# Optimization experiments

Hardware: AMD Instinct MI355X
Metric: run time of the kernel (lower is better)

## Reference

```python
import jax, jax.numpy as jnp
import numpy as np

DIM = 192
NUM_HEADS = 6
WS = (2, 8, 8)          # (wd, wh, ww)
SHIFT = (1, 4, 4)
B, D, H, W = 2, 4, 128, 128
N_WIN_TOK = WS[0] * WS[1] * WS[2]   # 128
NW = (D // WS[0]) * (H // WS[1]) * (W // WS[2])  # 512 windows per sample


def _rel_pos_index(ws):
    d, h, w = ws
    coords = np.stack(np.meshgrid(np.arange(d), np.arange(h), np.arange(w), indexing='ij'))
    cf = coords.reshape(3, -1)
    rel = (cf[:, :, None] - cf[:, None, :]).transpose(1, 2, 0).astype(np.int64)
    rel[:, :, 0] += d - 1
    rel[:, :, 1] += h - 1
    rel[:, :, 2] += w - 1
    rel[:, :, 0] *= (2 * h - 1) * (2 * w - 1)
    rel[:, :, 1] *= 2 * w - 1
    return rel.sum(-1)  # (N, N)

REL_IDX = _rel_pos_index(WS)


def _sine_pos(HW, num_pos_feats, temperature=10000.0):
    # matches get_sine_position_encoding(normalize=True)
    scale = 2 * np.pi
    eps = 1e-6
    ones = np.ones((1, HW[0], HW[1]), np.float32)
    y = ones.cumsum(1)
    x = ones.cumsum(2)
    y = y / (y[:, -1:, :] + eps) * scale
    x = x / (x[:, :, -1:] + eps) * scale
    i = np.arange(num_pos_feats, dtype=np.float32)
    dim_t = temperature ** (2.0 * np.floor(i / 2) / num_pos_feats)
    px = x[:, :, :, None] / dim_t
    py = y[:, :, :, None] / dim_t
    px = np.stack((np.sin(px[..., 0::2]), np.cos(px[..., 1::2])), axis=4).reshape(1, HW[0], HW[1], -1)
    py = np.stack((np.sin(py[..., 0::2]), np.cos(py[..., 1::2])), axis=4).reshape(1, HW[0], HW[1], -1)
    pos = np.concatenate((py, px), axis=3)  # (1, H, W, 2*npf)
    return pos.reshape(1, HW[0] * HW[1], -1)

POS_BIAS = _sine_pos((WS[1], WS[2]), DIM // 2)  # (1, 64, DIM)


def _ln(x, w, b):
    mu = x.mean(-1, keepdims=True)
    var = x.var(-1, keepdims=True)
    return (x - mu) / jnp.sqrt(var + 1e-5) * w + b


def _qkv(x, w, b):
    B_, N, C = x.shape
    y = (x @ w.T + b).reshape(B_, N, 3, NUM_HEADS, C // NUM_HEADS).transpose(2, 0, 3, 1, 4)
    return y[0], y[1], y[2]  # each (B_, h, N, hd)


def _attn(q, k, v, mask, rpb=None):
    # q,k,v: (B_, h, N, hd); mask: (nW, N, N) or None; rpb: (h, N, N) or None
    scale = q.shape[-1] ** -0.5
    a = jnp.einsum('bhnd,bhmd->bhnm', q * scale, k)
    if rpb is not None:
        a = a + rpb[None]
    if mask is not None:
        B_, h, N, _ = a.shape
        nW = mask.shape[0]
        a = (a.reshape(B_ // nW, nW, h, N, N) + mask[None, :, None]).reshape(B_, h, N, N)
    a = jax.nn.softmax(a, axis=-1)
    out = jnp.einsum('bhnm,bhmd->bhnd', a, v)
    B_, h, N, hd = out.shape
    return out.transpose(0, 2, 1, 3).reshape(B_, N, h * hd)


def setup_inputs() -> dict:
    key = jax.random.key(0)
    ks = jax.random.split(key, 8)
    C = DIM
    hid = int(C * 2.0)
    f = lambda k, shp: jax.random.normal(k, shp, jnp.float32) * 0.02
    tbl = (2 * WS[0] - 1) * (2 * WS[1] - 1) * (2 * WS[2] - 1)
    return {
        'x': jax.random.normal(ks[0], (B, D, H, W, C), jnp.float32),
        'mask_matrix': jnp.zeros((NW, N_WIN_TOK, N_WIN_TOK), jnp.float32),
        'norm1_w': jnp.ones((C,), jnp.float32), 'norm1_b': jnp.zeros((C,), jnp.float32),
        'qkv_self_w': f(ks[1], (3 * C, C)), 'qkv_self_b': jnp.zeros((3 * C,), jnp.float32),
        'qkv_mut_w': f(ks[2], (3 * C, C)), 'qkv_mut_b': jnp.zeros((3 * C,), jnp.float32),
        'rpb_table': f(ks[3], (tbl, NUM_HEADS)),
        'proj_w': f(ks[4], (C, 2 * C)), 'proj_b': jnp.zeros((C,), jnp.float32),
        'norm2_w': jnp.ones((C,), jnp.float32), 'norm2_b': jnp.zeros((C,), jnp.float32),
        'fc11_w': f(ks[5], (hid, C)), 'fc11_b': jnp.zeros((hid,), jnp.float32),
        'fc12_w': f(ks[6], (hid, C)), 'fc12_b': jnp.zeros((hid,), jnp.float32),
        'fc2_w': f(ks[7], (C, hid)), 'fc2_b': jnp.zeros((C,), jnp.float32),
    }


def reference(x, mask_matrix, norm1_w, norm1_b, qkv_self_w, qkv_self_b,
              qkv_mut_w, qkv_mut_b, rpb_table, proj_w, proj_b,
              norm2_w, norm2_b, fc11_w, fc11_b, fc12_w, fc12_b, fc2_w, fc2_b):
    Bb, Dd, Hh, Ww_, C = x.shape
    wd, wh, ww = WS
    N = wd * wh * ww
    Nh = N // 2

    # ---- part1: windowed mutual+self attention with cyclic shift ----
    h1 = _ln(x, norm1_w, norm1_b)
    sh = jnp.roll(h1, (-SHIFT[0], -SHIFT[1], -SHIFT[2]), axis=(1, 2, 3))
    # window_partition -> (B*nW, N, C)
    xw = sh.reshape(Bb, Dd // wd, wd, Hh // wh, wh, Ww_ // ww, ww, C)
    xw = xw.transpose(0, 1, 3, 5, 2, 4, 6, 7).reshape(-1, N, C)

    # self-attention with relative position bias
    q, k, v = _qkv(xw, qkv_self_w, qkv_self_b)
    rpb = rpb_table[REL_IDX.reshape(-1)].reshape(N, N, NUM_HEADS).transpose(2, 0, 1)
    x_self = _attn(q, k, v, mask_matrix[:, :N, :N], rpb)  # (B_, N, C)

    # mutual attention (no relative bias), sine positional bias added to input
    pos = jnp.tile(jnp.asarray(POS_BIAS, x.dtype), (1, 2, 1))  # (1, N, C)
    q, k, v = _qkv(xw + pos, qkv_mut_w, qkv_mut_b)
    q1, q2 = q[:, :, :Nh], q[:, :, Nh:]
    k1, k2 = k[:, :, :Nh], k[:, :, Nh:]
    v1, v2 = v[:, :, :Nh], v[:, :, Nh:]
    m2 = mask_matrix[:, :Nh, :Nh]
    x1 = _attn(q2, k1, v1, m2)  # frame2 queries attend frame1
    x2 = _attn(q1, k2, v2, m2)
    x_out = jnp.concatenate([jnp.concatenate([x1, x2], axis=1), x_self], axis=2)  # (B_, N, 2C)
    xp = x_out @ proj_w.T + proj_b  # (B_, N, C)

    # window_reverse + roll back
    rev = xp.reshape(Bb, Dd // wd, Hh // wh, Ww_ // ww, wd, wh, ww, C)
    rev = rev.transpose(0, 1, 4, 2, 5, 3, 6, 7).reshape(Bb, Dd, Hh, Ww_, C)
    rev = jnp.roll(rev, SHIFT, axis=(1, 2, 3))
    x = x + rev

    # ---- part2: GEGLU MLP ----
    h2 = _ln(x, norm2_w, norm2_b)
    mlp = (jax.nn.gelu(h2 @ fc11_w.T + fc11_b, approximate=False) * (h2 @ fc12_w.T + fc12_b)) @ fc2_w.T + fc2_b
    return x + mlp
```

## Files before the change

kernel.cpp:

```cpp
#include <hip/hip_runtime.h>
#include <hip/hip_bf16.h>

typedef __hip_bfloat16 bf16;
typedef __attribute__((ext_vector_type(8))) short short8;
typedef __attribute__((ext_vector_type(4))) float f32x4;

#define NTOKENS 131072
#define MFMA __builtin_amdgcn_mfma_f32_16x16x32_bf16

static constexpr size_t A_OFF    = 0;
static constexpr size_t Q_OFF    = A_OFF   + (size_t)NTOKENS*192*2;
static constexpr size_t O_OFF    = Q_OFF   + (size_t)NTOKENS*576*2;
static constexpr size_t POS_OFF  = O_OFF   + (size_t)NTOKENS*384*2;
static constexpr size_t PB_OFF   = POS_OFF + (size_t)128*192*4;
static constexpr size_t RPBF_OFF = PB_OFF  + (size_t)128*576*4;
static constexpr size_t MSKF_OFF = RPBF_OFF+ (size_t)6*128*128*2;
static constexpr size_t WB_OFF   = MSKF_OFF+ (size_t)512*128*128*2;
static constexpr size_t WQS_E = 0, WQM_E = 110592, WPR_E = 221184,
                        W11_E = 294912, W12_E = 368640, W2_E = 442368, WTOT = 516096;

__device__ __forceinline__ float u2f(unsigned int ubits) {
    union { unsigned int i; float f; } c; c.i = ubits << 16; return c.f;
}
__device__ __forceinline__ unsigned pkbf(float a, float b) {
    unsigned ua = (unsigned)__bfloat16_as_ushort(__float2bfloat16(a));
    unsigned ub = (unsigned)__bfloat16_as_ushort(__float2bfloat16(b));
    return ua | (ub << 16);
}
__device__ __forceinline__ unsigned swz(unsigned b) { return b ^ (((b >> 9) & 1) << 5); }
__device__ __forceinline__ short8 u4s8(uint4 v) { union { uint4 u; short8 s; } c; c.u = v; return c.s; }

__device__ __forceinline__ void gl16(const bf16* g, void* l) {
    __builtin_amdgcn_global_load_lds(
        (const __attribute__((address_space(1))) void*)g,
        (__attribute__((address_space(3))) void*)l, 16, 0, 0);
}

__global__ __launch_bounds__(256) void cvtw_kernel(
    const float* __restrict__ a, const float* __restrict__ b, const float* __restrict__ c,
    const float* __restrict__ d, const float* __restrict__ e, const float* __restrict__ f,
    bf16* __restrict__ out) {
    int i = blockIdx.x * 256 + threadIdx.x;
    const float* src; int off;
    if      (i < (int)WQM_E) { src = a; off = (int)WQS_E; }
    else if (i < (int)WPR_E) { src = b; off = (int)WQM_E; }
    else if (i < (int)W11_E) { src = c; off = (int)WPR_E; }
    else if (i < (int)W12_E) { src = d; off = (int)W11_E; }
    else if (i < (int)W2_E)  { src = e; off = (int)W12_E; }
    else if (i < (int)WTOT)  { src = f; off = (int)W2_E; }
    else return;
    out[i] = __float2bfloat16(src[i - off]);
}

__global__ __launch_bounds__(256) void pos_kernel(float* __restrict__ pos) {
    int idx = blockIdx.x * 256 + threadIdx.x;
    if (idx >= 128 * 192) return;
    int t = idx / 192, c = idx - t * 192;
    int s = t & 63;
    int hh = s >> 3, ww = s & 7;
    const float twopi = 6.2831853071795864f;
    float coord = (c < 96) ? (float)(hh + 1) : (float)(ww + 1);
    coord = coord / (8.0f + 1e-6f) * twopi;
    int f = (c < 96) ? c : c - 96;
    float dimt = powf(10000.0f, (float)(2 * (f >> 1)) / 96.0f);
    float v = coord / dimt;
    pos[idx] = (f & 1) ? cosf(v) : sinf(v);
}

__global__ __launch_bounds__(256) void pbias_kernel(const float* __restrict__ pos,
                                                    const bf16* __restrict__ Wm,
                                                    const float* __restrict__ bqm,
                                                    float* __restrict__ PB) {
    int idx = blockIdx.x * 256 + threadIdx.x;
    if (idx >= 128 * 576) return;
    int t = idx / 576, n = idx - t * 576;
    const float* pp = pos + t * 192;
    const bf16* wp = Wm + (size_t)n * 192;
    float acc = bqm[n];
    for (int k = 0; k < 192; ++k) acc += pp[k] * __bfloat162float(wp[k]);
    PB[idx] = acc;
}

__global__ __launch_bounds__(256) void rpbF_kernel(const float* __restrict__ tbl,
                                                   bf16* __restrict__ rpbF) {
    int idx = blockIdx.x * 256 + threadIdx.x;
    if (idx >= 6 * 32 * 128 * 4) return;
    int jr = idx & 3;
    int i = (idx >> 2) & 127;
    int jq = (idx >> 9) & 31;
    int h = idx >> 14;
    int j = jq * 4 + jr;
    int di = i >> 6, hi = (i >> 3) & 7, wi = i & 7;
    int dj = j >> 6, hj = (j >> 3) & 7, wj = j & 7;
    int t = (di - dj + 1) * 225 + (hi - hj + 7) * 15 + (wi - wj + 7);
    rpbF[idx] = __float2bfloat16(tbl[t * 6 + h]);
}

__global__ __launch_bounds__(256) void mskF_kernel(const float* __restrict__ mask,
                                                   bf16* __restrict__ mskF) {
    int idx = blockIdx.x * 256 + threadIdx.x;
    int widx = idx >> 12;
    int rem = idx & 4095;
    int i = rem >> 5, jq = rem & 31;
    float4 v = *reinterpret_cast<const float4*>(mask + ((size_t)widx << 14) + i * 128 + jq * 4);
    uint2 o;
    o.x = pkbf(v.x, v.y);
    o.y = pkbf(v.z, v.w);
    *reinterpret_cast<uint2*>(mskF + ((size_t)widx << 14) + (jq * 128 + i) * 4) = o;
}

template <int PART>
__global__ __launch_bounds__(256) void ln_kernel(const float* __restrict__ xin,
                                                 const float* __restrict__ w,
                                                 const float* __restrict__ b,
                                                 bf16* __restrict__ out) {
    int tok = blockIdx.x * 4 + (threadIdx.x >> 6);
    int lane = threadIdx.x & 63;
    const float* xp = xin + (size_t)tok * 192;
    float x0 = xp[lane], x1 = xp[lane + 64], x2 = xp[lane + 128];
    float s = x0 + x1 + x2;
    float ss = x0 * x0 + x1 * x1 + x2 * x2;
    for (int off = 32; off; off >>= 1) {
        s += __shfl_xor(s, off);
        ss += __shfl_xor(ss, off);
    }
    float mean = s * (1.0f / 192.0f);
    float var = ss * (1.0f / 192.0f) - mean * mean;
    float rstd = rsqrtf(var + 1e-5f);
    size_t obase;
    if (PART) {
        int bb = tok >> 16;
        int rem = tok & 65535;
        int d = rem >> 14;
        int hw = rem & 16383;
        int hh = hw >> 7, w2 = hw & 127;
        int sd = (d + 3) & 3;
        int sh = (hh + 124) & 127;
        int sw = (w2 + 124) & 127;
        int win = ((bb * 2 + (sd >> 1)) * 16 + (sh >> 3)) * 16 + (sw >> 3);
        int t = ((sd & 1) << 6) | ((sh & 7) << 3) | (sw & 7);
        obase = ((size_t)win * 128 + t) * 192;
    } else {
        obase = (size_t)tok * 192;
    }
    out[obase + lane]       = __float2bfloat16((x0 - mean) * rstd * w[lane] + b[lane]);
    out[obase + lane + 64]  = __float2bfloat16((x1 - mean) * rstd * w[lane + 64] + b[lane + 64]);
    out[obase + lane + 128] = __float2bfloat16((x2 - mean) * rstd * w[lane + 128] + b[lane + 128]);
}

template <int MODE, int BIAS>
__global__ __launch_bounds__(256) void mgemm(
    const bf16* __restrict__ Ab, int K, int nb,
    const bf16* __restrict__ W1, const float* __restrict__ B1,
    const bf16* __restrict__ W2, const float* __restrict__ B2,
    const float* __restrict__ resid,
    void* __restrict__ outp) {
    __shared__ __align__(16) unsigned char AsB[2][16384];
    __shared__ __align__(16) unsigned char WsB[2][8192];
    __shared__ __align__(16) unsigned char Ws2B[(MODE == 3) ? 2 : 1][(MODE == 3) ? 8192 : 16];

    int total = gridDim.x;
    int bid = blockIdx.x;
    int lin = (bid & 7) * (total >> 3) + (bid >> 3);
    int mb = lin / nb, nbk = lin - mb * nb;
    int m0 = mb << 7, n0 = nbk << 6;
    int tid = threadIdx.x;
    int w = tid >> 6, l = tid & 63;
    int wr = w >> 1, wc = w & 1;
    int lr = l & 15, lg = l >> 4;

    f32x4 acc[4][2] = {};
    f32x4 acc2[4][2] = {};

    auto stage = [&](int buf, int kc) {
        int k0 = kc << 6;
#pragma unroll
        for (int it = 0; it < 4; ++it) {
            int idx = it * 256 + tid;
            int row = idx >> 3, gs = idx & 7;
            int gsrc = gs ^ (((row >> 2) & 1) << 1);
            gl16(Ab + (size_t)(m0 + row) * K + k0 + gsrc * 8, &AsB[buf][idx * 16]);
        }
#pragma unroll
        for (int it = 0; it < 2; ++it) {
            int idx = it * 256 + tid;
            int row = idx >> 3, gs = idx & 7;
            int gsrc = gs ^ (((row >> 2) & 1) << 1);
            gl16(W1 + (size_t)(n0 + row) * K + k0 + gsrc * 8, &WsB[buf][idx * 16]);
            if (MODE == 3)
                gl16(W2 + (size_t)(n0 + row) * K + k0 + gsrc * 8, &Ws2B[buf][idx * 16]);
        }
    };

    int nK = K >> 6;
    stage(0, 0);
    __syncthreads();
    for (int kc = 0; kc < nK; ++kc) {
        int cur = kc & 1;
        if (kc + 1 < nK) stage(cur ^ 1, kc + 1);
        const unsigned char* as = AsB[cur];
        const unsigned char* wsb = WsB[cur];
        const unsigned char* ws2 = Ws2B[(MODE == 3) ? cur : 0];
#pragma unroll
        for (int ks = 0; ks < 2; ++ks) {
            short8 af[4], wf[2], wf2[2];
#pragma unroll
            for (int rb = 0; rb < 4; ++rb)
                af[rb] = *reinterpret_cast<const short8*>(
                    &as[swz((wr * 64 + rb * 16 + lr) * 128 + ks * 64 + lg * 16)]);
#pragma unroll
            for (int cb = 0; cb < 2; ++cb) {
                wf[cb] = *reinterpret_cast<const short8*>(
                    &wsb[swz((wc * 32 + cb * 16 + lr) * 128 + ks * 64 + lg * 16)]);
                if (MODE == 3)
                    wf2[cb] = *reinterpret_cast<const short8*>(
                        &ws2[swz((wc * 32 + cb * 16 + lr) * 128 + ks * 64 + lg * 16)]);
            }
#pragma unroll
            for (int rb = 0; rb < 4; ++rb)
#pragma unroll
                for (int cb = 0; cb < 2; ++cb) {
                    acc[rb][cb] = MFMA(af[rb], wf[cb], acc[rb][cb], 0, 0, 0);
                    if (MODE == 3) acc2[rb][cb] = MFMA(af[rb], wf2[cb], acc2[rb][cb], 0, 0, 0);
                }
        }
        __syncthreads();
    }

    if (MODE == 0 || MODE == 3) {
        bf16* eb = (bf16*)AsB[0];
#pragma unroll
        for (int rb = 0; rb < 4; ++rb)
#pragma unroll
            for (int r = 0; r < 4; ++r) {
                int ml = wr * 64 + rb * 16 + lg * 4 + r;
#pragma unroll
                for (int cb = 0; cb < 2; ++cb) {
                    int cl = wc * 32 + cb * 16 + lr;
                    int n = n0 + cl;
                    if (MODE == 0) {
                        float bias_v = BIAS ? resid[(ml & 127) * 576 + n] : B1[n];
                        eb[ml * 64 + cl] = __float2bfloat16(acc[rb][cb][r] + bias_v);
                    } else {
                        float u = acc[rb][cb][r] + B1[n];
                        float v2 = acc2[rb][cb][r] + B2[n];
                        float t = u * (0.7978845608028654f + 0.0356774081363001f * u * u);
                        float g = u * v2 / (1.0f + __expf(-2.0f * t));
                        eb[ml * 64 + cl] = __float2bfloat16(g);
                    }
                }
            }
        __syncthreads();
        bf16* Og = (bf16*)outp;
        const int ostr = (MODE == 0) ? 576 : 384;
#pragma unroll
        for (int it = 0; it < 4; ++it) {
            int idx = it * 256 + tid;
            int row = idx >> 3, g = idx & 7;
            uint4 v = *reinterpret_cast<const uint4*>(&eb[row * 64 + g * 8]);
            *reinterpret_cast<uint4*>(Og + (size_t)(m0 + row) * ostr + n0 + g * 8) = v;
        }
    } else {
#pragma unroll
        for (int rb = 0; rb < 4; ++rb) {
#pragma unroll
            for (int r = 0; r < 4; ++r) {
                int m = m0 + wr * 64 + rb * 16 + lg * 4 + r;
                if (MODE == 2) {
                    int win = m >> 7, t = m & 127;
                    int bb = win >> 9, rem = win & 511;
                    int sd = ((rem >> 8) << 1) | (t >> 6);
                    int sh = (((rem >> 4) & 15) << 3) | ((t >> 3) & 7);
                    int sw = ((rem & 15) << 3) | (t & 7);
                    int dq = (sd + 1) & 3;
                    int hq = (sh + 4) & 127;
                    int wq = (sw + 4) & 127;
                    size_t gb = ((((size_t)bb * 4 + dq) * 128 + hq) * 128 + wq) * 192;
                    float* Rr = (float*)outp;
#pragma unroll
                    for (int cb = 0; cb < 2; ++cb) {
                        int n = n0 + wc * 32 + cb * 16 + lr;
                        Rr[gb + n] = resid[gb + n] + acc[rb][cb][r] + B1[n];
                    }
                } else {
                    float* Og = (float*)outp;
#pragma unroll
                    for (int cb = 0; cb < 2; ++cb) {
                        int n = n0 + wc * 32 + cb * 16 + lr;
                        Og[(size_t)m * 192 + n] =
                            resid[(size_t)m * 192 + n] + acc[rb][cb][r] + B1[n];
                    }
                }
            }
        }
    }
}

__global__ __launch_bounds__(256) void attn_self(
    const bf16* __restrict__ Qb, const bf16* __restrict__ rpbF,
    const bf16* __restrict__ mskF, bf16* __restrict__ Ob) {
    __shared__ __align__(16) bf16 VtB[4096];
    __shared__ __align__(16) bf16 EpiB[4][1280];
    int bid = blockIdx.x;
    int lin = (bid & 7) * 768 + (bid >> 3);
    int widx = lin / 12, sub = lin - widx * 12;
    int h = sub % 6, b2 = sub / 6;
    int win = b2 * 512 + widx;
    int tid = threadIdx.x, w = tid >> 6, l = tid & 63;
    int lr = l & 15, lg = l >> 4;
    const float qscale = 0.17677669529663689f;
    size_t qbase = (size_t)win * 128 * 576 + h * 32;

#pragma unroll
    for (int it = 0; it < 16; ++it) {
        int idx = it * 256 + tid;
        int d = idx & 31, j = idx >> 5;
        bf16 v = Qb[qbase + (size_t)j * 576 + 384 + d];
        VtB[(d * 256 + (((j >> 3) ^ (d & 7)) << 4) + (j & 7) * 2) >> 1] = v;
    }

    uint4 kf[8], qf[2];
#pragma unroll
    for (int jb = 0; jb < 8; ++jb)
        kf[jb] = *reinterpret_cast<const uint4*>(Qb + qbase + (size_t)(jb * 16 + lr) * 576 + 192 + lg * 8);
    int i0 = w * 32;
#pragma unroll
    for (int ib = 0; ib < 2; ++ib)
        qf[ib] = *reinterpret_cast<const uint4*>(Qb + qbase + (size_t)(i0 + ib * 16 + lr) * 576 + lg * 8);
    f32x4 s[8][2] = {};
#pragma unroll
    for (int jb = 0; jb < 8; ++jb)
#pragma unroll
        for (int ib = 0; ib < 2; ++ib)
            s[jb][ib] = MFMA(u4s8(kf[jb]), u4s8(qf[ib]), s[jb][ib], 0, 0, 0);

    const bf16* rpF = rpbF + (size_t)h * 16384;
    const bf16* mpF = mskF + (size_t)widx * 16384;
#pragma unroll
    for (int jb = 0; jb < 8; ++jb) {
        int jq0 = jb * 4 + lg;
#pragma unroll
        for (int ib = 0; ib < 2; ++ib) {
            int il = i0 + ib * 16 + lr;
            uint2 rv = *reinterpret_cast<const uint2*>(rpF + (jq0 * 128 + il) * 4);
            uint2 mv = *reinterpret_cast<const uint2*>(mpF + (jq0 * 128 + il) * 4);
            s[jb][ib][0] = fmaf(s[jb][ib][0], qscale, u2f(rv.x & 0xffffu) + u2f(mv.x & 0xffffu));
            s[jb][ib][1] = fmaf(s[jb][ib][1], qscale, u2f(rv.x >> 16) + u2f(mv.x >> 16));
            s[jb][ib][2] = fmaf(s[jb][ib][2], qscale, u2f(rv.y & 0xffffu) + u2f(mv.y & 0xffffu));
            s[jb][ib][3] = fmaf(s[jb][ib][3], qscale, u2f(rv.y >> 16) + u2f(mv.y >> 16));
        }
    }

    float rs[2];
    unsigned w0[2][8], w1[2][8];
#pragma unroll
    for (int ib = 0; ib < 2; ++ib) {
        float mx = -1e30f;
#pragma unroll
        for (int jb = 0; jb < 8; ++jb)
#pragma unroll
            for (int r = 0; r < 4; ++r) mx = fmaxf(mx, s[jb][ib][r]);
        mx = fmaxf(mx, __shfl_xor(mx, 16));
        mx = fmaxf(mx, __shfl_xor(mx, 32));
        float sum = 0.0f;
#pragma unroll
        for (int jb = 0; jb < 8; ++jb)
#pragma unroll
            for (int r = 0; r < 4; ++r) {
                float e = __expf(s[jb][ib][r] - mx);
                s[jb][ib][r] = e;
                sum += e;
            }
        sum += __shfl_xor(sum, 16);
        sum += __shfl_xor(sum, 32);
        rs[ib] = 1.0f / sum;
#pragma unroll
        for (int jb = 0; jb < 8; ++jb) {
            w0[ib][jb] = pkbf(s[jb][ib][0], s[jb][ib][1]);
            w1[ib][jb] = pkbf(s[jb][ib][2], s[jb][ib][3]);
        }
    }
    __syncthreads();

    f32x4 o[2][2] = {};
    int srcA = lr + 16 * (2 * (lg & 1));
    int srcB = srcA + 16;
    bool hi = ((lg >> 1) & 1) != 0;
#pragma unroll
    for (int ks = 0; ks < 4; ++ks) {
        short8 vt[2];
#pragma unroll
        for (int db = 0; db < 2; ++db) {
            int d = db * 16 + lr;
            vt[db] = *reinterpret_cast<const short8*>(
                &VtB[(d * 256 + (((ks * 4 + lg) ^ (d & 7)) << 4)) >> 1]);
        }
#pragma unroll
        for (int ib = 0; ib < 2; ++ib) {
            unsigned xa0 = (unsigned)__shfl((int)w0[ib][2 * ks], srcA, 64);
            unsigned xa1 = (unsigned)__shfl((int)w0[ib][2 * ks + 1], srcA, 64);
            unsigned xb0 = (unsigned)__shfl((int)w1[ib][2 * ks], srcA, 64);
            unsigned xb1 = (unsigned)__shfl((int)w1[ib][2 * ks + 1], srcA, 64);
            unsigned xc0 = (unsigned)__shfl((int)w0[ib][2 * ks], srcB, 64);
            unsigned xc1 = (unsigned)__shfl((int)w0[ib][2 * ks + 1], srcB, 64);
            unsigned xd0 = (unsigned)__shfl((int)w1[ib][2 * ks], srcB, 64);
            unsigned xd1 = (unsigned)__shfl((int)w1[ib][2 * ks + 1], srcB, 64);
            uint4 bfv;
            bfv.x = hi ? xa1 : xa0;
            bfv.y = hi ? xb1 : xb0;
            bfv.z = hi ? xc1 : xc0;
            bfv.w = hi ? xd1 : xd0;
            short8 pb = u4s8(bfv);
#pragma unroll
            for (int db = 0; db < 2; ++db) o[db][ib] = MFMA(vt[db], pb, o[db][ib], 0, 0, 0);
        }
    }

    bf16* eb = &EpiB[w][0];
#pragma unroll
    for (int db = 0; db < 2; ++db)
#pragma unroll
        for (int ib = 0; ib < 2; ++ib)
#pragma unroll
            for (int r = 0; r < 4; ++r) {
                int d = db * 16 + lg * 4 + r;
                int il = ib * 16 + lr;
                eb[il * 40 + d] = __float2bfloat16(o[db][ib][r] * rs[ib]);
            }
    int il2 = l >> 1, hf = l & 1;
    uint4 oa = *reinterpret_cast<const uint4*>(&eb[il2 * 40 + hf * 16]);
    uint4 ob2 = *reinterpret_cast<const uint4*>(&eb[il2 * 40 + hf * 16 + 8]);
    size_t gbase = ((size_t)win * 128 + i0 + il2) * 384 + 192 + h * 32 + hf * 16;
    *reinterpret_cast<uint4*>(Ob + gbase) = oa;
    *reinterpret_cast<uint4*>(Ob + gbase + 8) = ob2;
}

__global__ __launch_bounds__(256) void attn_mut(
    const bf16* __restrict__ Qb, const bf16* __restrict__ mskF, bf16* __restrict__ Ob) {
    __shared__ __align__(16) bf16 VtB[4096];
    __shared__ __align__(16) bf16 EpiB[4][1280];
    int bid = blockIdx.x;
    int lin = (bid & 7) * 768 + (bid >> 3);
    int widx = lin / 12, sub = lin - widx * 12;
    int h = sub % 6, b2 = sub / 6;
    int win = b2 * 512 + widx;
    int tid = threadIdx.x, w = tid >> 6, l = tid & 63;
    int lr = l & 15, lg = l >> 4;
    const float qscale = 0.17677669529663689f;
    size_t qbase = (size_t)win * 128 * 576 + h * 32;

#pragma unroll
    for (int it = 0; it < 16; ++it) {
        int idx = it * 256 + tid;
        int d = idx & 31, j = idx >> 5;
        bf16 v = Qb[qbase + (size_t)j * 576 + 384 + d];
        VtB[(d * 256 + (((j >> 3) ^ (d & 7)) << 4) + (j & 7) * 2) >> 1] = v;
    }

    int i0 = w * 32;
    int qoff = (w < 2) ? 64 : -64;
    int koff = (w < 2) ? 0 : 64;
    uint4 kf[4], qf[2];
#pragma unroll
    for (int jb = 0; jb < 4; ++jb)
        kf[jb] = *reinterpret_cast<const uint4*>(
            Qb + qbase + (size_t)(koff + jb * 16 + lr) * 576 + 192 + lg * 8);
#pragma unroll
    for (int ib = 0; ib < 2; ++ib)
        qf[ib] = *reinterpret_cast<const uint4*>(
            Qb + qbase + (size_t)(i0 + ib * 16 + lr + qoff) * 576 + lg * 8);
    f32x4 s[4][2] = {};
#pragma unroll
    for (int jb = 0; jb < 4; ++jb)
#pragma unroll
        for (int ib = 0; ib < 2; ++ib)
            s[jb][ib] = MFMA(u4s8(kf[jb]), u4s8(qf[ib]), s[jb][ib], 0, 0, 0);

    const bf16* mpF = mskF + (size_t)widx * 16384;
    int ibase = (i0 & 63);
#pragma unroll
    for (int jb = 0; jb < 4; ++jb) {
        int jq0 = jb * 4 + lg;
#pragma unroll
        for (int ib = 0; ib < 2; ++ib) {
            int il = ibase + ib * 16 + lr;
            uint2 mv = *reinterpret_cast<const uint2*>(mpF + (jq0 * 128 + il) * 4);
            s[jb][ib][0] = fmaf(s[jb][ib][0], qscale, u2f(mv.x & 0xffffu));
            s[jb][ib][1] = fmaf(s[jb][ib][1], qscale, u2f(mv.x >> 16));
            s[jb][ib][2] = fmaf(s[jb][ib][2], qscale, u2f(mv.y & 0xffffu));
            s[jb][ib][3] = fmaf(s[jb][ib][3], qscale, u2f(mv.y >> 16));
        }
    }

    float rs[2];
    unsigned w0[2][4], w1[2][4];
#pragma unroll
    for (int ib = 0; ib < 2; ++ib) {
        float mx = -1e30f;
#pragma unroll
        for (int jb = 0; jb < 4; ++jb)
#pragma unroll
            for (int r = 0; r < 4; ++r) mx = fmaxf(mx, s[jb][ib][r]);
        mx = fmaxf(mx, __shfl_xor(mx, 16));
        mx = fmaxf(mx, __shfl_xor(mx, 32));
        float sum = 0.0f;
#pragma unroll
        for (int jb = 0; jb < 4; ++jb)
#pragma unroll
            for (int r = 0; r < 4; ++r) {
                float e = __expf(s[jb][ib][r] - mx);
                s[jb][ib][r] = e;
                sum += e;
            }
        sum += __shfl_xor(sum, 16);
        sum += __shfl_xor(sum, 32);
        rs[ib] = 1.0f / sum;
#pragma unroll
        for (int jb = 0; jb < 4; ++jb) {
            w0[ib][jb] = pkbf(s[jb][ib][0], s[jb][ib][1]);
            w1[ib][jb] = pkbf(s[jb][ib][2], s[jb][ib][3]);
        }
    }
    __syncthreads();

    f32x4 o[2][2] = {};
    int srcA = lr + 16 * (2 * (lg & 1));
    int srcB = srcA + 16;
    bool hi = ((lg >> 1) & 1) != 0;
    int gb0 = koff >> 3;
#pragma unroll
    for (int ks = 0; ks < 2; ++ks) {
        short8 vt[2];
#pragma unroll
        for (int db = 0; db < 2; ++db) {
            int d = db * 16 + lr;
            vt[db] = *reinterpret_cast<const short8*>(
                &VtB[(d * 256 + (((gb0 + ks * 4 + lg) ^ (d & 7)) << 4)) >> 1]);
        }
#pragma unroll
        for (int ib = 0; ib < 2; ++ib) {
            unsigned xa0 = (unsigned)__shfl((int)w0[ib][2 * ks], srcA, 64);
            unsigned xa1 = (unsigned)__shfl((int)w0[ib][2 * ks + 1], srcA, 64);
            unsigned xb0 = (unsigned)__shfl((int)w1[ib][2 * ks], srcA, 64);
            unsigned xb1 = (unsigned)__shfl((int)w1[ib][2 * ks + 1], srcA, 64);
            unsigned xc0 = (unsigned)__shfl((int)w0[ib][2 * ks], srcB, 64);
            unsigned xc1 = (unsigned)__shfl((int)w0[ib][2 * ks + 1], srcB, 64);
            unsigned xd0 = (unsigned)__shfl((int)w1[ib][2 * ks], srcB, 64);
            unsigned xd1 = (unsigned)__shfl((int)w1[ib][2 * ks + 1], srcB, 64);
            uint4 bfv;
            bfv.x = hi ? xa1 : xa0;
            bfv.y = hi ? xb1 : xb0;
            bfv.z = hi ? xc1 : xc0;
            bfv.w = hi ? xd1 : xd0;
            short8 pb = u4s8(bfv);
#pragma unroll
            for (int db = 0; db < 2; ++db) o[db][ib] = MFMA(vt[db], pb, o[db][ib], 0, 0, 0);
        }
    }

    bf16* eb = &EpiB[w][0];
#pragma unroll
    for (int db = 0; db < 2; ++db)
#pragma unroll
        for (int ib = 0; ib < 2; ++ib)
#pragma unroll
            for (int r = 0; r < 4; ++r) {
                int d = db * 16 + lg * 4 + r;
                int il = ib * 16 + lr;
                eb[il * 40 + d] = __float2bfloat16(o[db][ib][r] * rs[ib]);
            }
    int il2 = l >> 1, hf = l & 1;
    uint4 oa = *reinterpret_cast<const uint4*>(&eb[il2 * 40 + hf * 16]);
    uint4 ob2 = *reinterpret_cast<const uint4*>(&eb[il2 * 40 + hf * 16 + 8]);
    size_t gbase = ((size_t)win * 128 + i0 + il2) * 384 + h * 32 + hf * 16;
    *reinterpret_cast<uint4*>(Ob + gbase) = oa;
    *reinterpret_cast<uint4*>(Ob + gbase + 8) = ob2;
}

extern "C" void kernel_launch(void* const* d_in, const int* in_sizes, int n_in,
                              void* d_out, int out_size, void* d_ws, size_t ws_size,
                              hipStream_t stream) {
    const float* x    = (const float*)d_in[0];
    const float* mask = (const float*)d_in[1];
    const float* n1w  = (const float*)d_in[2];
    const float* n1b  = (const float*)d_in[3];
    const float* wqs  = (const float*)d_in[4];
    const float* bqs  = (const float*)d_in[5];
    const float* wqm  = (const float*)d_in[6];
    const float* bqm  = (const float*)d_in[7];
    const float* rpbt = (const float*)d_in[8];
    const float* wproj= (const float*)d_in[9];
    const float* bproj= (const float*)d_in[10];
    const float* n2w  = (const float*)d_in[11];
    const float* n2b  = (const float*)d_in[12];
    const float* w11  = (const float*)d_in[13];
    const float* b11  = (const float*)d_in[14];
    const float* w12  = (const float*)d_in[15];
    const float* b12  = (const float*)d_in[16];
    const float* w2   = (const float*)d_in[17];
    const float* b2   = (const float*)d_in[18];

    char* ws = (char*)d_ws;
    bf16*  A    = (bf16*)(ws + A_OFF);
    bf16*  Q    = (bf16*)(ws + Q_OFF);
    bf16*  O    = (bf16*)(ws + O_OFF);
    float* pos  = (float*)(ws + POS_OFF);
    float* PB   = (float*)(ws + PB_OFF);
    bf16*  rpbF = (bf16*)(ws + RPBF_OFF);
    bf16*  mskF = (bf16*)(ws + MSKF_OFF);
    bf16*  WB   = (bf16*)(ws + WB_OFF);
    bf16*  Hb = A;
    bf16*  G  = Q;
    float* R  = (float*)d_out;
    float* out = (float*)d_out;

    cvtw_kernel<<<(WTOT + 255) / 256, 256, 0, stream>>>(wqs, wqm, wproj, w11, w12, w2, WB);
    pos_kernel<<<96, 256, 0, stream>>>(pos);
    pbias_kernel<<<288, 256, 0, stream>>>(pos, WB + WQM_E, bqm, PB);
    rpbF_kernel<<<384, 256, 0, stream>>>(rpbt, rpbF);
    mskF_kernel<<<8192, 256, 0, stream>>>(mask, mskF);
    ln_kernel<1><<<32768, 256, 0, stream>>>(x, n1w, n1b, A);
    mgemm<0, 0><<<9 * 1024, 256, 0, stream>>>(A, 192, 9, WB + WQS_E, bqs, nullptr, nullptr,
                                              nullptr, Q);
    attn_self<<<6144, 256, 0, stream>>>(Q, rpbF, mskF, O);
    mgemm<0, 1><<<9 * 1024, 256, 0, stream>>>(A, 192, 9, WB + WQM_E, nullptr, nullptr, nullptr,
                                              PB, Q);
    attn_mut<<<6144, 256, 0, stream>>>(Q, mskF, O);
    mgemm<2, 0><<<3 * 1024, 256, 0, stream>>>(O, 384, 3, WB + WPR_E, bproj, nullptr, nullptr,
                                              x, R);
    ln_kernel<0><<<32768, 256, 0, stream>>>(R, n2w, n2b, Hb);
    mgemm<3, 0><<<6 * 1024, 256, 0, stream>>>(Hb, 192, 6, WB + W11_E, b11, WB + W12_E, b12,
                                              nullptr, G);
    mgemm<4, 0><<<3 * 1024, 256, 0, stream>>>(G, 384, 3, WB + W2_E, b2, nullptr, nullptr,
                                              R, out);
}
```

Measured before the change: 573.9 us.

## Load GEMM operands directly into registers instead of staging through LDS

The mgemm kernel no longer double-buffers A and W tiles through shared memory with global_load_lds. Each thread now preloads its whole weight fragment for the full K into registers and streams A fragments straight from global memory with a one-step register prefetch. K becomes a compile-time template parameter and occupancy hints are added through launch bounds. This drops LDS staging and the barriers, but it raises register pressure and gives up the coalesced, shared A loads, since each wave reads its own rows with 16-byte strided accesses.

```diff
diff --git a/kernel.cpp b/kernel.cpp
--- a/kernel.cpp
+++ b/kernel.cpp
@@ -27,14 +27,7 @@
     unsigned ub = (unsigned)__bfloat16_as_ushort(__float2bfloat16(b));
     return ua | (ub << 16);
 }
-__device__ __forceinline__ unsigned swz(unsigned b) { return b ^ (((b >> 9) & 1) << 5); }
 __device__ __forceinline__ short8 u4s8(uint4 v) { union { uint4 u; short8 s; } c; c.u = v; return c.s; }
-
-__device__ __forceinline__ void gl16(const bf16* g, void* l) {
-    __builtin_amdgcn_global_load_lds(
-        (const __attribute__((address_space(1))) void*)g,
-        (__attribute__((address_space(3))) void*)l, 16, 0, 0);
-}
 
 __global__ __launch_bounds__(256) void cvtw_kernel(
     const float* __restrict__ a, const float* __restrict__ b, const float* __restrict__ c,
@@ -148,16 +141,16 @@
     out[obase + lane + 128] = __float2bfloat16((x2 - mean) * rstd * w[lane + 128] + b[lane + 128]);
 }
 
-template <int MODE, int BIAS>
-__global__ __launch_bounds__(256) void mgemm(
-    const bf16* __restrict__ Ab, int K, int nb,
+template <int MODE, int BIAS, int NKS>
+__global__ __launch_bounds__(256, (MODE == 3 || NKS == 12) ? 2 : 3) void mgemm(
+    const bf16* __restrict__ Ab, int nb,
     const bf16* __restrict__ W1, const float* __restrict__ B1,
     const bf16* __restrict__ W2, const float* __restrict__ B2,
     const float* __restrict__ resid,
     void* __restrict__ outp) {
-    __shared__ __align__(16) unsigned char AsB[2][16384];
-    __shared__ __align__(16) unsigned char WsB[2][8192];
-    __shared__ __align__(16) unsigned char Ws2B[(MODE == 3) ? 2 : 1][(MODE == 3) ? 8192 : 16];
+    constexpr int K = NKS * 32;
+    constexpr bool DUAL = (MODE == 3);
+    __shared__ __align__(16) bf16 eb[128 * 64];
 
     int total = gridDim.x;
     int bid = blockIdx.x;
@@ -169,66 +162,55 @@
     int wr = w >> 1, wc = w & 1;
     int lr = l & 15, lg = l >> 4;
 
+    const bf16* wrow = W1 + (size_t)(n0 + wc * 32 + lr) * K + lg * 8;
+    uint4 wf[2][NKS];
+#pragma unroll
+    for (int cb = 0; cb < 2; ++cb)
+#pragma unroll
+        for (int kk = 0; kk < NKS; ++kk)
+            wf[cb][kk] = *reinterpret_cast<const uint4*>(wrow + cb * 16 * K + kk * 32);
+    uint4 wf2[DUAL ? 2 : 1][DUAL ? NKS : 1];
+    if (DUAL) {
+        const bf16* wrow2 = W2 + (size_t)(n0 + wc * 32 + lr) * K + lg * 8;
+#pragma unroll
+        for (int cb = 0; cb < 2; ++cb)
+#pragma unroll
+            for (int kk = 0; kk < NKS; ++kk)
+                wf2[cb][kk] = *reinterpret_cast<const uint4*>(wrow2 + cb * 16 * K + kk * 32);
+    }
+
+    const bf16* arow = Ab + (size_t)(m0 + wr * 64 + lr) * K + lg * 8;
+
     f32x4 acc[4][2] = {};
     f32x4 acc2[4][2] = {};
 
-    auto stage = [&](int buf, int kc) {
-        int k0 = kc << 6;
-#pragma unroll
-        for (int it = 0; it < 4; ++it) {
-            int idx = it * 256 + tid;
-            int row = idx >> 3, gs = idx & 7;
-            int gsrc = gs ^ (((row >> 2) & 1) << 1);
-            gl16(Ab + (size_t)(m0 + row) * K + k0 + gsrc * 8, &AsB[buf][idx * 16]);
-        }
-#pragma unroll
-        for (int it = 0; it < 2; ++it) {
-            int idx = it * 256 + tid;
-            int row = idx >> 3, gs = idx & 7;
-            int gsrc = gs ^ (((row >> 2) & 1) << 1);
-            gl16(W1 + (size_t)(n0 + row) * K + k0 + gsrc * 8, &WsB[buf][idx * 16]);
-            if (MODE == 3)
-                gl16(W2 + (size_t)(n0 + row) * K + k0 + gsrc * 8, &Ws2B[buf][idx * 16]);
-        }
-    };
-
-    int nK = K >> 6;
-    stage(0, 0);
-    __syncthreads();
-    for (int kc = 0; kc < nK; ++kc) {
-        int cur = kc & 1;
-        if (kc + 1 < nK) stage(cur ^ 1, kc + 1);
-        const unsigned char* as = AsB[cur];
-        const unsigned char* wsb = WsB[cur];
-        const unsigned char* ws2 = Ws2B[(MODE == 3) ? cur : 0];
-#pragma unroll
-        for (int ks = 0; ks < 2; ++ks) {
-            short8 af[4], wf[2], wf2[2];
+    uint4 af[4];
+#pragma unroll
+    for (int rb = 0; rb < 4; ++rb)
+        af[rb] = *reinterpret_cast<const uint4*>(arow + rb * 16 * K);
+#pragma unroll
+    for (int kk = 0; kk < NKS; ++kk) {
+        uint4 afn[4];
+        if (kk + 1 < NKS) {
 #pragma unroll
             for (int rb = 0; rb < 4; ++rb)
-                af[rb] = *reinterpret_cast<const short8*>(
-                    &as[swz((wr * 64 + rb * 16 + lr) * 128 + ks * 64 + lg * 16)]);
+                afn[rb] = *reinterpret_cast<const uint4*>(arow + rb * 16 * K + (kk + 1) * 32);
+        }
+#pragma unroll
+        for (int rb = 0; rb < 4; ++rb)
 #pragma unroll
             for (int cb = 0; cb < 2; ++cb) {
-                wf[cb] = *reinterpret_cast<const short8*>(
-                    &wsb[swz((wc * 32 + cb * 16 + lr) * 128 + ks * 64 + lg * 16)]);
-                if (MODE == 3)
-                    wf2[cb] = *reinterpret_cast<const short8*>(
-                        &ws2[swz((wc * 32 + cb * 16 + lr) * 128 + ks * 64 + lg * 16)]);
+                acc[rb][cb] = MFMA(u4s8(af[rb]), u4s8(wf[cb][kk]), acc[rb][cb], 0, 0, 0);
+                if (DUAL)
+                    acc2[rb][cb] = MFMA(u4s8(af[rb]), u4s8(wf2[cb][kk]), acc2[rb][cb], 0, 0, 0);
             }
-#pragma unroll
-            for (int rb = 0; rb < 4; ++rb)
-#pragma unroll
-                for (int cb = 0; cb < 2; ++cb) {
-                    acc[rb][cb] = MFMA(af[rb], wf[cb], acc[rb][cb], 0, 0, 0);
-                    if (MODE == 3) acc2[rb][cb] = MFMA(af[rb], wf2[cb], acc2[rb][cb], 0, 0, 0);
-                }
-        }
-        __syncthreads();
+        if (kk + 1 < NKS) {
+#pragma unroll
+            for (int rb = 0; rb < 4; ++rb) af[rb] = afn[rb];
+        }
     }
 
     if (MODE == 0 || MODE == 3) {
-        bf16* eb = (bf16*)AsB[0];
 #pragma unroll
         for (int rb = 0; rb < 4; ++rb)
 #pragma unroll
@@ -620,17 +602,17 @@
     rpbF_kernel<<<384, 256, 0, stream>>>(rpbt, rpbF);
     mskF_kernel<<<8192, 256, 0, stream>>>(mask, mskF);
     ln_kernel<1><<<32768, 256, 0, stream>>>(x, n1w, n1b, A);
-    mgemm<0, 0><<<9 * 1024, 256, 0, stream>>>(A, 192, 9, WB + WQS_E, bqs, nullptr, nullptr,
-                                              nullptr, Q);
+    mgemm<0, 0, 6><<<9 * 1024, 256, 0, stream>>>(A, 9, WB + WQS_E, bqs, nullptr, nullptr,
+                                                 nullptr, Q);
     attn_self<<<6144, 256, 0, stream>>>(Q, rpbF, mskF, O);
-    mgemm<0, 1><<<9 * 1024, 256, 0, stream>>>(A, 192, 9, WB + WQM_E, nullptr, nullptr, nullptr,
-                                              PB, Q);
+    mgemm<0, 1, 6><<<9 * 1024, 256, 0, stream>>>(A, 9, WB + WQM_E, nullptr, nullptr, nullptr,
+                                                 PB, Q);
     attn_mut<<<6144, 256, 0, stream>>>(Q, mskF, O);
-    mgemm<2, 0><<<3 * 1024, 256, 0, stream>>>(O, 384, 3, WB + WPR_E, bproj, nullptr, nullptr,
-                                              x, R);
+    mgemm<2, 0, 12><<<3 * 1024, 256, 0, stream>>>(O, 3, WB + WPR_E, bproj, nullptr, nullptr,
+                                                  x, R);
     ln_kernel<0><<<32768, 256, 0, stream>>>(R, n2w, n2b, Hb);
-    mgemm<3, 0><<<6 * 1024, 256, 0, stream>>>(Hb, 192, 6, WB + W11_E, b11, WB + W12_E, b12,
-                                              nullptr, G);
-    mgemm<4, 0><<<3 * 1024, 256, 0, stream>>>(G, 384, 3, WB + W2_E, b2, nullptr, nullptr,
-                                              R, out);
-}
+    mgemm<3, 0, 6><<<6 * 1024, 256, 0, stream>>>(Hb, 6, WB + W11_E, b11, WB + W12_E, b12,
+                                                 nullptr, G);
+    mgemm<4, 0, 12><<<3 * 1024, 256, 0, stream>>>(G, 3, WB + W2_E, b2, nullptr, nullptr,
+                                                  R, out);
+}
```

After: 905.1 us. 57.7% more time.

## Deepen GEMM global-to-LDS prefetch to two stages with explicit vmcnt waits

Applied to the files above, without the earlier changes.

The GEMM main loop now issues loads for the first two K-chunks up front. Each iteration waits with a counted s_waitcnt vmcnt, so it blocks only on the current chunk while the next chunk's loads stay in flight. The buffer just consumed is refilled with chunk kc+2 after an LDS-read drain and barrier. This hides more global-memory latency behind the MFMA work. In exchange it relies on hand-coded vmcnt values that must match the exact number of gl16 loads each stage issues, and it adds a second barrier per iteration.

```diff
diff --git a/kernel.cpp b/kernel.cpp
--- a/kernel.cpp
+++ b/kernel.cpp
@@ -155,9 +155,10 @@
     const bf16* __restrict__ W2, const float* __restrict__ B2,
     const float* __restrict__ resid,
     void* __restrict__ outp) {
+    constexpr bool DUAL = (MODE == 3);
     __shared__ __align__(16) unsigned char AsB[2][16384];
     __shared__ __align__(16) unsigned char WsB[2][8192];
-    __shared__ __align__(16) unsigned char Ws2B[(MODE == 3) ? 2 : 1][(MODE == 3) ? 8192 : 16];
+    __shared__ __align__(16) unsigned char Ws2B[DUAL ? 2 : 1][DUAL ? 8192 : 16];
 
     int total = gridDim.x;
     int bid = blockIdx.x;
@@ -187,20 +188,28 @@
             int row = idx >> 3, gs = idx & 7;
             int gsrc = gs ^ (((row >> 2) & 1) << 1);
             gl16(W1 + (size_t)(n0 + row) * K + k0 + gsrc * 8, &WsB[buf][idx * 16]);
-            if (MODE == 3)
+            if (DUAL)
                 gl16(W2 + (size_t)(n0 + row) * K + k0 + gsrc * 8, &Ws2B[buf][idx * 16]);
         }
     };
 
     int nK = K >> 6;
     stage(0, 0);
-    __syncthreads();
+    stage(1, 1);
     for (int kc = 0; kc < nK; ++kc) {
+        if (kc < nK - 1) {
+            if constexpr (DUAL) asm volatile("s_waitcnt vmcnt(8)" ::: "memory");
+            else                asm volatile("s_waitcnt vmcnt(6)" ::: "memory");
+        } else {
+            asm volatile("s_waitcnt vmcnt(0)" ::: "memory");
+        }
+        __builtin_amdgcn_s_barrier();
+        __builtin_amdgcn_sched_barrier(0);
+
         int cur = kc & 1;
-        if (kc + 1 < nK) stage(cur ^ 1, kc + 1);
         const unsigned char* as = AsB[cur];
         const unsigned char* wsb = WsB[cur];
-        const unsigned char* ws2 = Ws2B[(MODE == 3) ? cur : 0];
+        const unsigned char* ws2 = Ws2B[DUAL ? cur : 0];
 #pragma unroll
         for (int ks = 0; ks < 2; ++ks) {
             short8 af[4], wf[2], wf2[2];
@@ -212,7 +221,7 @@
             for (int cb = 0; cb < 2; ++cb) {
                 wf[cb] = *reinterpret_cast<const short8*>(
                     &wsb[swz((wc * 32 + cb * 16 + lr) * 128 + ks * 64 + lg * 16)]);
-                if (MODE == 3)
+                if (DUAL)
                     wf2[cb] = *reinterpret_cast<const short8*>(
                         &ws2[swz((wc * 32 + cb * 16 + lr) * 128 + ks * 64 + lg * 16)]);
             }
@@ -221,11 +230,20 @@
 #pragma unroll
                 for (int cb = 0; cb < 2; ++cb) {
                     acc[rb][cb] = MFMA(af[rb], wf[cb], acc[rb][cb], 0, 0, 0);
-                    if (MODE == 3) acc2[rb][cb] = MFMA(af[rb], wf2[cb], acc2[rb][cb], 0, 0, 0);
+                    if (DUAL) acc2[rb][cb] = MFMA(af[rb], wf2[cb], acc2[rb][cb], 0, 0, 0);
                 }
         }
-        __syncthreads();
-    }
+
+        if (kc + 2 < nK) {
+            asm volatile("s_waitcnt lgkmcnt(0)" ::: "memory");
+            __builtin_amdgcn_s_barrier();
+            __builtin_amdgcn_sched_barrier(0);
+            stage(cur, kc + 2);
+        }
+    }
+    asm volatile("s_waitcnt lgkmcnt(0)" ::: "memory");
+    __builtin_amdgcn_s_barrier();
+    __builtin_amdgcn_sched_barrier(0);
 
     if (MODE == 0 || MODE == 3) {
         bf16* eb = (bf16*)AsB[0];
```

Result: no change. 576.9 us (+0.5%).

## Load GEMM weight fragments directly into registers instead of staging via LDS

Applied to the files above, without the earlier changes.

The GEMM kernel no longer stages the weight tile through shared memory. Each lane now loads its MFMA B-fragments straight from global memory into registers, with a one-step register prefetch for the next K chunk. The A-tile LDS swizzle also changes to a full 8-way XOR on row&7 to cut bank conflicts. This lowers LDS use and LDS traffic, which may raise occupancy, but it adds register pressure and uncoalesced global weight loads, especially in the dual-weight mode.

```diff
diff --git a/kernel.cpp b/kernel.cpp
--- a/kernel.cpp
+++ b/kernel.cpp
@@ -27,7 +27,6 @@
     unsigned ub = (unsigned)__bfloat16_as_ushort(__float2bfloat16(b));
     return ua | (ub << 16);
 }
-__device__ __forceinline__ unsigned swz(unsigned b) { return b ^ (((b >> 9) & 1) << 5); }
 __device__ __forceinline__ short8 u4s8(uint4 v) { union { uint4 u; short8 s; } c; c.u = v; return c.s; }
 
 __device__ __forceinline__ void gl16(const bf16* g, void* l) {
@@ -155,9 +154,8 @@
     const bf16* __restrict__ W2, const float* __restrict__ B2,
     const float* __restrict__ resid,
     void* __restrict__ outp) {
+    constexpr bool DUAL = (MODE == 3);
     __shared__ __align__(16) unsigned char AsB[2][16384];
-    __shared__ __align__(16) unsigned char WsB[2][8192];
-    __shared__ __align__(16) unsigned char Ws2B[(MODE == 3) ? 2 : 1][(MODE == 3) ? 8192 : 16];
 
     int total = gridDim.x;
     int bid = blockIdx.x;
@@ -178,53 +176,73 @@
         for (int it = 0; it < 4; ++it) {
             int idx = it * 256 + tid;
             int row = idx >> 3, gs = idx & 7;
-            int gsrc = gs ^ (((row >> 2) & 1) << 1);
+            int gsrc = gs ^ (row & 7);
             gl16(Ab + (size_t)(m0 + row) * K + k0 + gsrc * 8, &AsB[buf][idx * 16]);
         }
-#pragma unroll
-        for (int it = 0; it < 2; ++it) {
-            int idx = it * 256 + tid;
-            int row = idx >> 3, gs = idx & 7;
-            int gsrc = gs ^ (((row >> 2) & 1) << 1);
-            gl16(W1 + (size_t)(n0 + row) * K + k0 + gsrc * 8, &WsB[buf][idx * 16]);
-            if (MODE == 3)
-                gl16(W2 + (size_t)(n0 + row) * K + k0 + gsrc * 8, &Ws2B[buf][idx * 16]);
-        }
     };
+
+    const bf16* wbase  = W1 + (size_t)(n0 + wc * 32 + lr) * K + lg * 8;
+    const bf16* wbase2 = DUAL ? (W2 + (size_t)(n0 + wc * 32 + lr) * K + lg * 8) : wbase;
+
+    uint4 wcur[2][2], wnxt[2][2];
+    uint4 wcur2[2][2], wnxt2[2][2];
 
     int nK = K >> 6;
     stage(0, 0);
+#pragma unroll
+    for (int cb = 0; cb < 2; ++cb)
+#pragma unroll
+        for (int ks = 0; ks < 2; ++ks) {
+            wcur[cb][ks] = *reinterpret_cast<const uint4*>(wbase + (size_t)cb * 16 * K + ks * 32);
+            if constexpr (DUAL)
+                wcur2[cb][ks] = *reinterpret_cast<const uint4*>(wbase2 + (size_t)cb * 16 * K + ks * 32);
+        }
     __syncthreads();
     for (int kc = 0; kc < nK; ++kc) {
         int cur = kc & 1;
-        if (kc + 1 < nK) stage(cur ^ 1, kc + 1);
+        if (kc + 1 < nK) {
+            stage(cur ^ 1, kc + 1);
+            int ko = (kc + 1) * 64;
+#pragma unroll
+            for (int cb = 0; cb < 2; ++cb)
+#pragma unroll
+                for (int ks = 0; ks < 2; ++ks) {
+                    wnxt[cb][ks] = *reinterpret_cast<const uint4*>(
+                        wbase + (size_t)cb * 16 * K + ko + ks * 32);
+                    if constexpr (DUAL)
+                        wnxt2[cb][ks] = *reinterpret_cast<const uint4*>(
+                            wbase2 + (size_t)cb * 16 * K + ko + ks * 32);
+                }
+        }
         const unsigned char* as = AsB[cur];
-        const unsigned char* wsb = WsB[cur];
-        const unsigned char* ws2 = Ws2B[(MODE == 3) ? cur : 0];
 #pragma unroll
         for (int ks = 0; ks < 2; ++ks) {
-            short8 af[4], wf[2], wf2[2];
+            short8 af[4];
+#pragma unroll
+            for (int rb = 0; rb < 4; ++rb) {
+                int row = wr * 64 + rb * 16 + lr;
+                af[rb] = *reinterpret_cast<const short8*>(
+                    &as[(unsigned)((row * 128 + ks * 64 + lg * 16) ^ ((row & 7) << 4))]);
+            }
 #pragma unroll
             for (int rb = 0; rb < 4; ++rb)
-                af[rb] = *reinterpret_cast<const short8*>(
-                    &as[swz((wr * 64 + rb * 16 + lr) * 128 + ks * 64 + lg * 16)]);
-#pragma unroll
-            for (int cb = 0; cb < 2; ++cb) {
-                wf[cb] = *reinterpret_cast<const short8*>(
-                    &wsb[swz((wc * 32 + cb * 16 + lr) * 128 + ks * 64 + lg * 16)]);
-                if (MODE == 3)
-                    wf2[cb] = *reinterpret_cast<const short8*>(
-                        &ws2[swz((wc * 32 + cb * 16 + lr) * 128 + ks * 64 + lg * 16)]);
-            }
-#pragma unroll
-            for (int rb = 0; rb < 4; ++rb)
 #pragma unroll
                 for (int cb = 0; cb < 2; ++cb) {
-                    acc[rb][cb] = MFMA(af[rb], wf[cb], acc[rb][cb], 0, 0, 0);
-                    if (MODE == 3) acc2[rb][cb] = MFMA(af[rb], wf2[cb], acc2[rb][cb], 0, 0, 0);
+                    acc[rb][cb] = MFMA(af[rb], u4s8(wcur[cb][ks]), acc[rb][cb], 0, 0, 0);
+                    if constexpr (DUAL)
+                        acc2[rb][cb] = MFMA(af[rb], u4s8(wcur2[cb][ks]), acc2[rb][cb], 0, 0, 0);
                 }
         }
         __syncthreads();
+        if (kc + 1 < nK) {
+#pragma unroll
+            for (int cb = 0; cb < 2; ++cb)
+#pragma unroll
+                for (int ks = 0; ks < 2; ++ks) {
+                    wcur[cb][ks] = wnxt[cb][ks];
+                    if constexpr (DUAL) wcur2[cb][ks] = wnxt2[cb][ks];
+                }
+        }
     }
 
     if (MODE == 0 || MODE == 3) {
```

Result: slower. 633.2 us (+10.3%).
